# Kernel optimization log

Measured on AMD Instinct MI355X. Metric: run time of the kernel, lower is better.

## Reference

```python
import jax, jax.numpy as jnp
import numpy as np

V, D, H, L, T_CTX = 50257, 768, 12, 12, 1024
HD = D // H
GELU_C = float(np.sqrt(2.0 / np.pi))


def new_gelu(x):
    return 0.5 * x * (1.0 + jnp.tanh(GELU_C * (x + 0.044715 * x ** 3)))


def layernorm(x, w, b, eps=1e-5):
    mu = jnp.mean(x, axis=-1, keepdims=True)
    var = jnp.var(x, axis=-1, keepdims=True)
    return (x - mu) * jax.lax.rsqrt(var + eps) * w + b


def setup_inputs() -> dict:
    key = jax.random.key(0)
    ks = jax.random.split(key, 20)
    B, T = 2, 1024
    s = 0.02
    inp = {
        "idx": jax.random.randint(ks[0], (B, T), 0, V),
        "targets": jax.random.randint(ks[1], (B, T), 0, V),
        "wte": jax.random.normal(ks[2], (V, D), jnp.float32) * s,
        "wpe": jax.random.normal(ks[3], (T_CTX, D), jnp.float32) * s,
        "ln1_w": jnp.ones((L, D)), "ln1_b": jnp.zeros((L, D)),
        "qkv_w": jax.random.normal(ks[4], (L, D, 3 * D), jnp.float32) * s,
        "qkv_b": jnp.zeros((L, 3 * D)),
        "proj_w": jax.random.normal(ks[5], (L, D, D), jnp.float32) * s,
        "proj_b": jnp.zeros((L, D)),
        "ln2_w": jnp.ones((L, D)), "ln2_b": jnp.zeros((L, D)),
        "fc_w": jax.random.normal(ks[6], (L, D, 4 * D), jnp.float32) * s,
        "fc_b": jnp.zeros((L, 4 * D)),
        "fc2_w": jax.random.normal(ks[7], (L, 4 * D, D), jnp.float32) * s,
        "fc2_b": jnp.zeros((L, D)),
        "lnf_w": jnp.ones((D,)), "lnf_b": jnp.zeros((D,)),
    }
    return inp


def _gpt_forward(idx, targets, wte, wpe, ln1_w, ln1_b, qkv_w, qkv_b, proj_w,
                 proj_b, ln2_w, ln2_b, fc_w, fc_b, fc2_w, fc2_b, lnf_w, lnf_b):
    B, T = idx.shape
    x = wte[idx] + wpe[:T]  # [B,T,D]
    scale = 1.0 / np.sqrt(HD)
    causal = jnp.tril(jnp.ones((T, T), dtype=bool))

    def block(x, p):
        l1w, l1b, qw, qb, pw, pb, l2w, l2b, fw, fb, f2w, f2b = p
        h = layernorm(x, l1w, l1b)
        qkv = h @ qw + qb  # [B,T,3D]
        q, k, v = jnp.split(qkv, 3, axis=-1)
        q = q.reshape(B, T, H, HD).transpose(0, 2, 1, 3)
        k = k.reshape(B, T, H, HD).transpose(0, 2, 1, 3)
        v = v.reshape(B, T, H, HD).transpose(0, 2, 1, 3)
        attn = jnp.einsum('bhqd,bhkd->bhqk', q, k) * scale
        attn = jnp.where(causal, attn, -jnp.inf)
        attn = jax.nn.softmax(attn, axis=-1)
        o = jnp.einsum('bhqk,bhkd->bhqd', attn, v)
        o = o.transpose(0, 2, 1, 3).reshape(B, T, D)
        x = x + (o @ pw + pb)
        h = layernorm(x, l2w, l2b)
        h = new_gelu(h @ fw + fb) @ f2w + f2b
        return x + h, None

    params = (ln1_w, ln1_b, qkv_w, qkv_b, proj_w, proj_b,
              ln2_w, ln2_b, fc_w, fc_b, fc2_w, fc2_b)
    x, _ = jax.lax.scan(block, x, params)
    x = layernorm(x, lnf_w, lnf_b)
    logits = x @ wte.T  # tied lm_head, [B,T,V]

    logp = jax.nn.log_softmax(logits, axis=-1)
    tflat = targets.reshape(-1)
    valid = tflat != -1
    tsafe = jnp.where(valid, tflat, 0)
    nll = -jnp.take_along_axis(logp.reshape(-1, V), tsafe[:, None], axis=-1)[:, 0]
    loss = jnp.sum(jnp.where(valid, nll, 0.0)) / jnp.maximum(jnp.sum(valid), 1)
    return logits, loss


def reference(idx, targets, wte, wpe, ln1_w, ln1_b, qkv_w, qkv_b, proj_w,
              proj_b, ln2_w, ln2_b, fc_w, fc_b, fc2_w, fc2_b, lnf_w, lnf_b):
    return _gpt_forward(idx, targets, wte, wpe, ln1_w, ln1_b, qkv_w, qkv_b,
                        proj_w, proj_b, ln2_w, ln2_b, fc_w, fc_b, fc2_w, fc2_b,
                        lnf_w, lnf_b)
```

## Files before the change

### kernel.cpp

```cpp
#include <hip/hip_runtime.h>
#include <hip/hip_bf16.h>
#include <math.h>

#define TT 1024
#define BB 2
#define DD 768
#define HH 12
#define NHD 64
#define LL 12
#define VV 50257
#define MROWS (BB*TT)
#define VPAD 50304
#define NT 393
#define NROWS (MROWS*HH)

typedef __attribute__((ext_vector_type(4))) float f32x4;
typedef __attribute__((ext_vector_type(8))) __bf16 bf16x8;
typedef __attribute__((ext_vector_type(8))) unsigned short u16x8;
typedef __hip_bfloat16 bf16;

__device__ __forceinline__ void gload_lds16(const bf16* g, bf16* l) {
    __builtin_amdgcn_global_load_lds((const __attribute__((address_space(1))) void*)g,
                                     (__attribute__((address_space(3))) void*)l, 16, 0, 0);
}

__global__ void embed_kernel(const int* __restrict__ idx, const float* __restrict__ wte,
                             const float* __restrict__ wpe, float* __restrict__ x) {
    int m = blockIdx.x;
    int t = m % TT;
    int tok = idx[m];
    const float* wrow = wte + (size_t)tok * DD;
    const float* prow = wpe + (size_t)t * DD;
    float* xrow = x + (size_t)m * DD;
    for (int c = threadIdx.x; c < DD; c += blockDim.x)
        xrow[c] = wrow[c] + prow[c];
}

__global__ void ln_kernel(const float* __restrict__ x, const float* __restrict__ w,
                          const float* __restrict__ b, bf16* __restrict__ out) {
    __shared__ float red[256];
    int m = blockIdx.x;
    int tid = threadIdx.x;
    const float* xr = x + (size_t)m * DD;
    float v0 = xr[tid], v1 = xr[tid + 256], v2 = xr[tid + 512];
    red[tid] = v0 + v1 + v2;
    __syncthreads();
    for (int s = 128; s > 0; s >>= 1) { if (tid < s) red[tid] += red[tid + s]; __syncthreads(); }
    float mu = red[0] * (1.0f / DD);
    __syncthreads();
    float d0 = v0 - mu, d1 = v1 - mu, d2 = v2 - mu;
    red[tid] = d0 * d0 + d1 * d1 + d2 * d2;
    __syncthreads();
    for (int s = 128; s > 0; s >>= 1) { if (tid < s) red[tid] += red[tid + s]; __syncthreads(); }
    float rstd = rsqrtf(red[0] * (1.0f / DD) + 1e-5f);
    bf16* orow = out + (size_t)m * DD;
    orow[tid]       = __float2bfloat16(d0 * rstd * w[tid]       + b[tid]);
    orow[tid + 256] = __float2bfloat16(d1 * rstd * w[tid + 256] + b[tid + 256]);
    orow[tid + 512] = __float2bfloat16(d2 * rstd * w[tid + 512] + b[tid + 512]);
}

__global__ void redln_kernel(const float* __restrict__ part, const float* __restrict__ bias,
                             const float* __restrict__ w, const float* __restrict__ b,
                             float* __restrict__ x, bf16* __restrict__ hb) {
    __shared__ float red[256];
    const size_t MN = (size_t)MROWS * DD;
    int m = blockIdx.x;
    int tid = threadIdx.x;
    float v[3];
    #pragma unroll
    for (int j = 0; j < 3; ++j) {
        int c = tid + j * 256;
        size_t i = (size_t)m * DD + c;
        v[j] = x[i] + part[i] + part[MN + i] + bias[c];
        x[i] = v[j];
    }
    red[tid] = v[0] + v[1] + v[2];
    __syncthreads();
    for (int s = 128; s > 0; s >>= 1) { if (tid < s) red[tid] += red[tid + s]; __syncthreads(); }
    float mu = red[0] * (1.0f / DD);
    __syncthreads();
    float d0 = v[0] - mu, d1 = v[1] - mu, d2 = v[2] - mu;
    red[tid] = d0 * d0 + d1 * d1 + d2 * d2;
    __syncthreads();
    for (int s = 128; s > 0; s >>= 1) { if (tid < s) red[tid] += red[tid + s]; __syncthreads(); }
    float rstd = rsqrtf(red[0] * (1.0f / DD) + 1e-5f);
    bf16* orow = hb + (size_t)m * DD;
    orow[tid]       = __float2bfloat16(d0 * rstd * w[tid]       + b[tid]);
    orow[tid + 256] = __float2bfloat16(d1 * rstd * w[tid + 256] + b[tid + 256]);
    orow[tid + 512] = __float2bfloat16(d2 * rstd * w[tid + 512] + b[tid + 512]);
}

__global__ void cast_kernel(const float* __restrict__ src, bf16* __restrict__ dst, int n4) {
    int stride = gridDim.x * blockDim.x;
    for (int i = blockIdx.x * blockDim.x + threadIdx.x; i < n4; i += stride) {
        float4 v = *(const float4*)(src + (size_t)i * 4);
        bf16* d = dst + (size_t)i * 4;
        d[0] = __float2bfloat16(v.x); d[1] = __float2bfloat16(v.y);
        d[2] = __float2bfloat16(v.z); d[3] = __float2bfloat16(v.w);
    }
}

__global__ void padzero_kernel(bf16* __restrict__ p, int n) {
    int i = blockIdx.x * 256 + threadIdx.x;
    if (i < n) p[i] = __float2bfloat16(0.f);
}

__global__ void tcast_kernel(const float* __restrict__ W, bf16* __restrict__ Wt,
                             int K, int N, size_t wstride, size_t tstride) {
    W  += (size_t)blockIdx.z * wstride;
    Wt += (size_t)blockIdx.z * tstride;
    __shared__ float t[32][33];
    int n0 = blockIdx.x * 32, k0 = blockIdx.y * 32;
    int c = threadIdx.x & 31, g = threadIdx.x >> 5;
    #pragma unroll
    for (int i = 0; i < 4; ++i) {
        int k = g * 4 + i;
        t[k][c] = W[(size_t)(k0 + k) * N + n0 + c];
    }
    __syncthreads();
    #pragma unroll
    for (int i = 0; i < 4; ++i) {
        int n = g * 4 + i;
        Wt[(size_t)(n0 + n) * K + k0 + c] = __float2bfloat16(t[c][n]);
    }
}

template<int BM, int BN, bool BIAS, bool GELU_, bool RES, bool OUTBF16, bool SPLITK>
__global__ __launch_bounds__(256, 3) void mgemm(
        const bf16* __restrict__ A, const bf16* __restrict__ Bm,
        const float* __restrict__ bias, const float* __restrict__ res,
        float* __restrict__ Cf, bf16* __restrict__ Cb, int M, int N, int K) {
    constexpr int WM = BM / 32, WN = BN / 32;
    constexpr int RA = BM / 32, RB = BN / 32;
    constexpr int NL = RA + RB;
    __shared__ __align__(16) bf16 As[2][BM * 64];
    __shared__ __align__(16) bf16 Bs[2][BN * 64];
    const int tid = threadIdx.x, lane = tid & 63, wid = tid >> 6;
    const int nbx = gridDim.x;
    const int nwg = nbx * gridDim.y;
    const int bidl = blockIdx.x + nbx * blockIdx.y;
    const int cpx = nwg >> 3;
    const int sw = (bidl & 7) * cpx + (bidl >> 3);
    const int m0 = (sw % nbx) * BM, n0 = (sw / nbx) * BN;
    const int wr = (wid >> 1) * (BM / 2), wc = (wid & 1) * (BN / 2);
    const int fr = lane & 15, fq = lane >> 4;

    const int Keff  = SPLITK ? (K >> 1) : K;
    const int kbase = SPLITK ? blockIdx.z * Keff : 0;
    if (SPLITK) Cf += (size_t)blockIdx.z * M * N;

    const int srow = tid >> 3;
    const int sk   = ((tid & 7) ^ (srow & 7)) * 8;
    const bf16* gA = A  + (size_t)(m0 + srow) * K + kbase + sk;
    const bf16* gB = Bm + (size_t)(n0 + srow) * K + kbase + sk;

    const int nt = Keff / 64;
    f32x4 acc[WM][WN] = {};

    auto stage = [&](int t) {
        bf16* dA = &As[t & 1][0] + tid * 8;
        bf16* dB = &Bs[t & 1][0] + tid * 8;
        const bf16* pA = gA + t * 64;
        const bf16* pB = gB + t * 64;
        #pragma unroll
        for (int u = 0; u < RA; ++u) gload_lds16(pA + (size_t)(u * 32) * K, dA + u * 2048);
        #pragma unroll
        for (int u = 0; u < RB; ++u) gload_lds16(pB + (size_t)(u * 32) * K, dB + u * 2048);
    };

    stage(0);

    for (int t = 0; t < nt; ++t) {
        if (t + 1 < nt) {
            stage(t + 1);
            asm volatile("s_waitcnt vmcnt(%0)" :: "i"(NL) : "memory");
        } else {
            asm volatile("s_waitcnt vmcnt(0)" ::: "memory");
        }
        __builtin_amdgcn_s_barrier();
        __builtin_amdgcn_sched_barrier(0);
        const bf16* abase = &As[t & 1][0];
        const bf16* bbase = &Bs[t & 1][0];
        #pragma unroll
        for (int ks = 0; ks < 2; ++ks) {
            const int kp = ((ks * 4 + fq) ^ (fr & 7)) * 8;
            bf16x8 af[WM], bq[WN];
            #pragma unroll
            for (int m = 0; m < WM; ++m)
                af[m] = *(const bf16x8*)(abase + (wr + m * 16 + fr) * 64 + kp);
            #pragma unroll
            for (int n = 0; n < WN; ++n)
                bq[n] = *(const bf16x8*)(bbase + (wc + n * 16 + fr) * 64 + kp);
            #pragma unroll
            for (int m = 0; m < WM; ++m)
                #pragma unroll
                for (int n = 0; n < WN; ++n)
                    acc[m][n] = __builtin_amdgcn_mfma_f32_16x16x32_bf16(af[m], bq[n], acc[m][n], 0, 0, 0);
        }
        __builtin_amdgcn_sched_barrier(0);
        __builtin_amdgcn_s_barrier();
    }

    #pragma unroll
    for (int m = 0; m < WM; ++m) {
        const int row = m0 + wr + m * 16 + fq * 4;
        #pragma unroll
        for (int n = 0; n < WN; ++n) {
            const int col = n0 + wc + n * 16 + fr;
            float bv = BIAS ? bias[col] : 0.f;
            #pragma unroll
            for (int r = 0; r < 4; ++r) {
                float v = acc[m][n][r] + bv;
                if (GELU_) {
                    float u = v;
                    float z = 1.5957691216057308f * (u + 0.044715f * u * u * u);
                    v = u / (1.0f + __expf(-z));
                }
                if (RES) v += res[(size_t)(row + r) * N + col];
                if (OUTBF16) Cb[(size_t)(row + r) * N + col] = __float2bfloat16(v);
                else         Cf[(size_t)(row + r) * N + col] = v;
            }
        }
    }
}

__global__ __launch_bounds__(512, 4) void mgemmL(
        const bf16* __restrict__ A, const bf16* __restrict__ Bm,
        float* __restrict__ Cf, float2* __restrict__ P, int N, int K) {
    constexpr int NL = 3;
    __shared__ __align__(16) bf16 As[2][256 * 32];
    __shared__ __align__(16) bf16 Bs[2][128 * 32];
    __shared__ float2 lbuf[8][64];
    const int tid = threadIdx.x, lane = tid & 63, wid = tid >> 6;
    const int nbx = gridDim.x;
    const int nwg = nbx * gridDim.y;
    const int bidl = blockIdx.x + nbx * blockIdx.y;
    const int cpx = nwg >> 3;
    const int sw = (bidl & 7) * cpx + (bidl >> 3);
    const int m0 = (sw % nbx) * 256, n0 = (sw / nbx) * 128;
    const int wm = wid >> 1, wn = wid & 1;
    const int wr = wm * 64, wc = wn * 64;
    const int fr = lane & 15, fq = lane >> 4;

    const int srow = tid >> 2;
    const int ksrc = ((tid & 3) ^ ((tid >> 3) & 3)) * 8;
    const bf16* gA = A  + (size_t)(m0 + srow) * K + ksrc;
    const bf16* gB = Bm + (size_t)(n0 + srow) * K + ksrc;
    const int kph = (fq ^ ((fr >> 1) & 3)) * 8;

    f32x4 acc[4][4] = {};
    const int nt = K / 32;

    auto stage = [&](int t) {
        bf16* dA = &As[t & 1][0] + tid * 8;
        bf16* dB = &Bs[t & 1][0] + tid * 8;
        const bf16* pA = gA + t * 32;
        #pragma unroll
        for (int u = 0; u < 2; ++u) gload_lds16(pA + (size_t)(u * 128) * K, dA + u * 4096);
        gload_lds16(gB + t * 32, dB);
    };

    stage(0);

    for (int t = 0; t < nt; ++t) {
        if (t + 1 < nt) {
            stage(t + 1);
            asm volatile("s_waitcnt vmcnt(%0)" :: "i"(NL) : "memory");
        } else {
            asm volatile("s_waitcnt vmcnt(0)" ::: "memory");
        }
        __builtin_amdgcn_s_barrier();
        __builtin_amdgcn_sched_barrier(0);
        const bf16* abase = &As[t & 1][0];
        const bf16* bbase = &Bs[t & 1][0];
        bf16x8 af[4], bq[4];
        #pragma unroll
        for (int m = 0; m < 4; ++m)
            af[m] = *(const bf16x8*)(abase + (wr + m * 16 + fr) * 32 + kph);
        #pragma unroll
        for (int n = 0; n < 4; ++n)
            bq[n] = *(const bf16x8*)(bbase + (wc + n * 16 + fr) * 32 + kph);
        #pragma unroll
        for (int m = 0; m < 4; ++m)
            #pragma unroll
            for (int n = 0; n < 4; ++n)
                acc[m][n] = __builtin_amdgcn_mfma_f32_16x16x32_bf16(af[m], bq[n], acc[m][n], 0, 0, 0);
        __builtin_amdgcn_sched_barrier(0);
        __builtin_amdgcn_s_barrier();
    }

    #pragma unroll
    for (int m = 0; m < 4; ++m) {
        const int row = m0 + wr + m * 16 + fq * 4;
        #pragma unroll
        for (int n = 0; n < 4; ++n) {
            const int col = n0 + wc + n * 16 + fr;
            if (col < N) {
                #pragma unroll
                for (int r = 0; r < 4; ++r)
                    Cf[(size_t)(row + r) * N + col] = acc[m][n][r];
            }
        }
    }
    #pragma unroll
    for (int m = 0; m < 4; ++m) {
        #pragma unroll
        for (int r = 0; r < 4; ++r) {
            float mx = -1e30f;
            #pragma unroll
            for (int n = 0; n < 4; ++n) {
                int col = n0 + wc + n * 16 + fr;
                mx = fmaxf(mx, (col < N) ? acc[m][n][r] : -1e30f);
            }
            #pragma unroll
            for (int msk = 1; msk <= 8; msk <<= 1) mx = fmaxf(mx, __shfl_xor(mx, msk));
            float sm = 0.f;
            #pragma unroll
            for (int n = 0; n < 4; ++n) {
                int col = n0 + wc + n * 16 + fr;
                if (col < N) sm += __expf(acc[m][n][r] - mx);
            }
            #pragma unroll
            for (int msk = 1; msk <= 8; msk <<= 1) sm += __shfl_xor(sm, msk);
            if (fr == 0) lbuf[wid][m * 16 + fq * 4 + r] = make_float2(mx, sm);
        }
    }
    __syncthreads();
    if (tid < 256) {
        int band = tid >> 6, rl = tid & 63;
        float2 a = lbuf[band * 2][rl];
        float2 b = lbuf[band * 2 + 1][rl];
        float mc = fmaxf(a.x, b.x);
        float sc = a.y * __expf(a.x - mc) + b.y * __expf(b.x - mc);
        P[(size_t)(m0 + band * 64 + rl) * NT + (n0 >> 7)] = make_float2(mc, sc);
    }
}

__global__ __launch_bounds__(256) void attn3_kernel(const bf16* __restrict__ qkv,
                                                    float* __restrict__ po,
                                                    float2* __restrict__ pml) {
    __shared__ bf16 Vt[64 * 64];
    __shared__ bf16 Ps[4][16 * 64];
    const int bid = blockIdx.x;
    const int z = blockIdx.y;
    const int q0 = (15 - (bid & 15)) * 64;
    const int h  = (bid / (TT / 64)) % HH;
    const int b  = bid / ((TT / 64) * HH);
    const int tid = threadIdx.x, lane = tid & 63, wid = tid >> 6;
    const int fr = lane & 15, fq = lane >> 4;
    const size_t rs = 3 * DD;

    const int nt_all = q0 / 64 + 1;
    const int lo = z ? (nt_all + 1) / 2 : 0;
    const int hi = z ? nt_all : (nt_all + 1) / 2;

    po  += (size_t)z * MROWS * DD;
    pml += (size_t)z * NROWS;

    if (lo >= hi) {
        #pragma unroll
        for (int r = 0; r < 4; ++r) {
            int q = q0 + wid * 16 + fq * 4 + r;
            size_t pidx = ((size_t)(b * TT + q) * HH + h);
            #pragma unroll
            for (int n2 = 0; n2 < 4; ++n2)
                po[pidx * NHD + n2 * 16 + fr] = 0.f;
            if (fr == 0) pml[pidx] = make_float2(-1e30f, 0.f);
        }
        return;
    }

    bf16x8 qf[2];
    {
        const bf16* qb = qkv + (size_t)(b * TT + q0 + wid * 16 + fr) * rs + h * NHD;
        qf[0] = *(const bf16x8*)(qb + fq * 8);
        qf[1] = *(const bf16x8*)(qb + 32 + fq * 8);
    }
    float mrun[4] = {-1e30f, -1e30f, -1e30f, -1e30f};
    float lrun[4] = {0.f, 0.f, 0.f, 0.f};
    f32x4 o[4] = {};
    const int vrow = (tid & 31) * 2, kq = tid >> 5;

    for (int jt = lo; jt < hi; ++jt) {
        __syncthreads();
        {
            const u16x8* vb = (const u16x8*)(qkv + (size_t)(b * TT + jt * 64 + vrow) * rs + 2 * DD + h * NHD + kq * 8);
            u16x8 v0 = vb[0];
            u16x8 v1 = *(const u16x8*)((const bf16*)vb + rs);
            #pragma unroll
            for (int j = 0; j < 8; ++j) {
                int d = kq * 8 + j;
                int e = (d * 64 + vrow) ^ ((d & 7) << 3);
                *(unsigned int*)&Vt[e] = (unsigned int)v0[j] | ((unsigned int)v1[j] << 16);
            }
        }
        f32x4 s[4] = {};
        const bf16* kb = qkv + (size_t)(b * TT + jt * 64 + fr) * rs + DD + h * NHD;
        __builtin_amdgcn_s_setprio(1);
        #pragma unroll
        for (int n = 0; n < 4; ++n) {
            bf16x8 k0 = *(const bf16x8*)(kb + (size_t)(n * 16) * rs + fq * 8);
            bf16x8 k1 = *(const bf16x8*)(kb + (size_t)(n * 16) * rs + 32 + fq * 8);
            s[n] = __builtin_amdgcn_mfma_f32_16x16x32_bf16(qf[0], k0, s[n], 0, 0, 0);
            s[n] = __builtin_amdgcn_mfma_f32_16x16x32_bf16(qf[1], k1, s[n], 0, 0, 0);
        }
        __builtin_amdgcn_s_setprio(0);
        float mt[4] = {-1e30f, -1e30f, -1e30f, -1e30f};
        #pragma unroll
        for (int n = 0; n < 4; ++n) {
            int colg = jt * 64 + n * 16 + fr;
            #pragma unroll
            for (int r = 0; r < 4; ++r) {
                int rowg = q0 + wid * 16 + fq * 4 + r;
                float v = s[n][r] * 0.125f;
                if (colg > rowg) v = -1e30f;
                s[n][r] = v;
                mt[r] = fmaxf(mt[r], v);
            }
        }
        #pragma unroll
        for (int msk = 1; msk <= 8; msk <<= 1)
            #pragma unroll
            for (int r = 0; r < 4; ++r) mt[r] = fmaxf(mt[r], __shfl_xor(mt[r], msk));
        float sc[4], pt[4] = {0.f, 0.f, 0.f, 0.f};
        #pragma unroll
        for (int r = 0; r < 4; ++r) {
            float mn = fmaxf(mrun[r], mt[r]);
            sc[r] = __expf(mrun[r] - mn);
            mrun[r] = mn;
        }
        #pragma unroll
        for (int n = 0; n < 4; ++n)
            #pragma unroll
            for (int r = 0; r < 4; ++r) {
                float p = __expf(s[n][r] - mrun[r]);
                s[n][r] = p;
                pt[r] += p;
            }
        #pragma unroll
        for (int msk = 1; msk <= 8; msk <<= 1)
            #pragma unroll
            for (int r = 0; r < 4; ++r) pt[r] += __shfl_xor(pt[r], msk);
        #pragma unroll
        for (int r = 0; r < 4; ++r) lrun[r] = lrun[r] * sc[r] + pt[r];
        #pragma unroll
        for (int n2 = 0; n2 < 4; ++n2)
            #pragma unroll
            for (int r = 0; r < 4; ++r) o[n2][r] *= sc[r];
        #pragma unroll
        for (int n = 0; n < 4; ++n)
            #pragma unroll
            for (int r = 0; r < 4; ++r) {
                int row = fq * 4 + r;
                int e = (row * 64 + n * 16 + fr) ^ ((row & 7) << 3);
                Ps[wid][e] = __float2bfloat16(s[n][r]);
            }
        __syncthreads();
        __builtin_amdgcn_s_setprio(1);
        #pragma unroll
        for (int ks = 0; ks < 2; ++ks) {
            int pe = (fr * 64 + ks * 32 + fq * 8) ^ ((fr & 7) << 3);
            bf16x8 pa = *(const bf16x8*)&Ps[wid][pe];
            #pragma unroll
            for (int n2 = 0; n2 < 4; ++n2) {
                int d = n2 * 16 + fr;
                int ve = (d * 64 + ks * 32 + fq * 8) ^ ((d & 7) << 3);
                bf16x8 vv = *(const bf16x8*)&Vt[ve];
                o[n2] = __builtin_amdgcn_mfma_f32_16x16x32_bf16(pa, vv, o[n2], 0, 0, 0);
            }
        }
        __builtin_amdgcn_s_setprio(0);
    }
    #pragma unroll
    for (int r = 0; r < 4; ++r) {
        int q = q0 + wid * 16 + fq * 4 + r;
        size_t pidx = ((size_t)(b * TT + q) * HH + h);
        #pragma unroll
        for (int n2 = 0; n2 < 4; ++n2)
            po[pidx * NHD + n2 * 16 + fr] = o[n2][r];
        if (fr == 0) pml[pidx] = make_float2(mrun[r], lrun[r]);
    }
}

__global__ void attn_combine(const float* __restrict__ po, const float2* __restrict__ pml,
                             bf16* __restrict__ out) {
    const size_t ZO = (size_t)MROWS * DD;
    int tid = threadIdx.x;
    size_t pidx = (size_t)blockIdx.x * 4 + (tid >> 6);
    int d = tid & 63;
    float2 a = pml[pidx];
    float2 b = pml[NROWS + pidx];
    float mt = fmaxf(a.x, b.x);
    float e0 = __expf(a.x - mt), e1 = __expf(b.x - mt);
    float l = a.y * e0 + b.y * e1;
    float ov = po[pidx * NHD + d] * e0 + po[ZO + pidx * NHD + d] * e1;
    int h = (int)(pidx % HH);
    size_t bt = pidx / HH;
    out[bt * DD + h * NHD + d] = __float2bfloat16(ov / l);
}

__global__ void zero_kernel(float* p) { if (threadIdx.x == 0) p[0] = 0.f; }

__global__ void loss_finish(const float2* __restrict__ P, const float* __restrict__ logits,
                            const int* __restrict__ targets, float* __restrict__ acc) {
    __shared__ float rm[256], rs[256];
    int m = blockIdx.x;
    int tid = threadIdx.x;
    float mx = -1e30f, sm = 0.f;
    for (int i = tid; i < NT; i += 256) {
        float2 p = P[(size_t)m * NT + i];
        float nm = fmaxf(mx, p.x);
        sm = sm * __expf(mx - nm) + p.y * __expf(p.x - nm);
        mx = nm;
    }
    rm[tid] = mx; rs[tid] = sm;
    __syncthreads();
    for (int s = 128; s > 0; s >>= 1) {
        if (tid < s) {
            float m2 = rm[tid + s], s2 = rs[tid + s];
            float nm = fmaxf(rm[tid], m2);
            rs[tid] = rs[tid] * __expf(rm[tid] - nm) + s2 * __expf(m2 - nm);
            rm[tid] = nm;
        }
        __syncthreads();
    }
    if (tid == 0) {
        float lse = logf(rs[0]) + rm[0];
        atomicAdd(acc, lse - logits[(size_t)m * VV + targets[m]]);
    }
}

__global__ void loss_final(const float* __restrict__ acc, float* __restrict__ out) {
    if (threadIdx.x == 0) out[0] = acc[0] * (1.0f / (float)MROWS);
}

extern "C" void kernel_launch(void* const* d_in, const int* in_sizes, int n_in,
                              void* d_out, int out_size, void* d_ws, size_t ws_size,
                              hipStream_t stream) {
    const int*   idx     = (const int*)d_in[0];
    const int*   targets = (const int*)d_in[1];
    const float* wte     = (const float*)d_in[2];
    const float* wpe     = (const float*)d_in[3];
    const float* ln1_w   = (const float*)d_in[4];
    const float* ln1_b   = (const float*)d_in[5];
    const float* qkv_w   = (const float*)d_in[6];
    const float* qkv_b   = (const float*)d_in[7];
    const float* proj_w  = (const float*)d_in[8];
    const float* proj_b  = (const float*)d_in[9];
    const float* ln2_w   = (const float*)d_in[10];
    const float* ln2_b   = (const float*)d_in[11];
    const float* fc_w    = (const float*)d_in[12];
    const float* fc_b    = (const float*)d_in[13];
    const float* fc2_w   = (const float*)d_in[14];
    const float* fc2_b   = (const float*)d_in[15];
    const float* lnf_w   = (const float*)d_in[16];
    const float* lnf_b   = (const float*)d_in[17];

    float* logits = (float*)d_out;
    float* loss_out = logits + (size_t)MROWS * VV;

    const size_t LQ = (size_t)3 * DD * DD, LP = (size_t)DD * DD;
    const size_t LF = (size_t)4 * DD * DD, LF2 = (size_t)4 * DD * DD;
    const size_t LSTRIDE = LQ + LP + LF + LF2;

    float* x    = (float*)d_ws;
    float* lacc = x + (size_t)MROWS * DD;
    float* part = lacc + 16;
    float2* pml = (float2*)(part + (size_t)2 * MROWS * DD);
    bf16* qkvbuf = (bf16*)(pml + (size_t)2 * NROWS);
    bf16* hb   = qkvbuf + (size_t)MROWS * 3 * DD;
    bf16* ab   = hb + (size_t)MROWS * DD;
    bf16* gb   = ab + (size_t)MROWS * DD;
    bf16* wteb = gb + (size_t)MROWS * 4 * DD;
    bf16* wbase = wteb + (size_t)VPAD * DD;

    const size_t fixed_bytes = (size_t)((char*)wbase - (char*)d_ws);
    const bool hoist = ws_size >= fixed_bytes + sizeof(bf16) * LSTRIDE * LL;

    dim3 blk(256);
    cast_kernel<<<2048, blk, 0, stream>>>(wte, wteb, VV * DD / 4);
    padzero_kernel<<<((VPAD - VV) * DD + 255) / 256, blk, 0, stream>>>(
        wteb + (size_t)VV * DD, (VPAD - VV) * DD);
    embed_kernel<<<MROWS, blk, 0, stream>>>(idx, wte, wpe, x);

    if (hoist) {
        tcast_kernel<<<dim3(3 * DD / 32, DD / 32, LL), blk, 0, stream>>>(
            qkv_w, wbase, DD, 3 * DD, LQ, LSTRIDE);
        tcast_kernel<<<dim3(DD / 32, DD / 32, LL), blk, 0, stream>>>(
            proj_w, wbase + LQ, DD, DD, LP, LSTRIDE);
        tcast_kernel<<<dim3(4 * DD / 32, DD / 32, LL), blk, 0, stream>>>(
            fc_w, wbase + LQ + LP, DD, 4 * DD, LF, LSTRIDE);
        tcast_kernel<<<dim3(DD / 32, 4 * DD / 32, LL), blk, 0, stream>>>(
            fc2_w, wbase + LQ + LP + LF, 4 * DD, DD, LF2, LSTRIDE);
    }

    ln_kernel<<<MROWS, blk, 0, stream>>>(x, ln1_w, ln1_b, hb);

    for (int l = 0; l < LL; ++l) {
        bf16* wl = hoist ? wbase + (size_t)l * LSTRIDE : wbase;
        bf16* wQT = wl, *wPT = wl + LQ, *wFT = wl + LQ + LP, *wF2T = wl + LQ + LP + LF;
        if (!hoist) {
            tcast_kernel<<<dim3(3 * DD / 32, DD / 32, 1), blk, 0, stream>>>(qkv_w + (size_t)l * LQ, wQT, DD, 3 * DD, 0, 0);
            tcast_kernel<<<dim3(DD / 32, DD / 32, 1), blk, 0, stream>>>(proj_w + (size_t)l * LP, wPT, DD, DD, 0, 0);
            tcast_kernel<<<dim3(4 * DD / 32, DD / 32, 1), blk, 0, stream>>>(fc_w + (size_t)l * LF, wFT, DD, 4 * DD, 0, 0);
            tcast_kernel<<<dim3(DD / 32, 4 * DD / 32, 1), blk, 0, stream>>>(fc2_w + (size_t)l * LF2, wF2T, 4 * DD, DD, 0, 0);
        }

        mgemm<128, 64, true, false, false, true, false><<<dim3(MROWS / 128, 3 * DD / 64), blk, 0, stream>>>(
            hb, wQT, qkv_b + (size_t)l * 3 * DD, nullptr, nullptr, qkvbuf, MROWS, 3 * DD, DD);

        attn3_kernel<<<dim3(BB * HH * (TT / 64), 2), blk, 0, stream>>>(qkvbuf, part, pml);
        attn_combine<<<NROWS / 4, blk, 0, stream>>>(part, pml, ab);

        mgemm<64, 64, false, false, false, false, true><<<dim3(MROWS / 64, DD / 64, 2), blk, 0, stream>>>(
            ab, wPT, nullptr, nullptr, part, nullptr, MROWS, DD, DD);
        redln_kernel<<<MROWS, blk, 0, stream>>>(part, proj_b + (size_t)l * DD,
            ln2_w + (size_t)l * DD, ln2_b + (size_t)l * DD, x, hb);

        mgemm<128, 64, true, true, false, true, false><<<dim3(MROWS / 128, 4 * DD / 64), blk, 0, stream>>>(
            hb, wFT, fc_b + (size_t)l * 4 * DD, nullptr, nullptr, gb, MROWS, 4 * DD, DD);

        mgemm<64, 64, false, false, false, false, true><<<dim3(MROWS / 64, DD / 64, 2), blk, 0, stream>>>(
            gb, wF2T, nullptr, nullptr, part, nullptr, MROWS, DD, 4 * DD);
        const float* nw = (l + 1 < LL) ? ln1_w + (size_t)(l + 1) * DD : lnf_w;
        const float* nb = (l + 1 < LL) ? ln1_b + (size_t)(l + 1) * DD : lnf_b;
        redln_kernel<<<MROWS, blk, 0, stream>>>(part, fc2_b + (size_t)l * DD, nw, nb, x, hb);
    }

    mgemmL<<<dim3(MROWS / 256, VPAD / 128), dim3(512), 0, stream>>>(
        hb, wteb, logits, (float2*)part, VV, DD);

    zero_kernel<<<1, 64, 0, stream>>>(lacc);
    loss_finish<<<MROWS, blk, 0, stream>>>((const float2*)part, logits, targets, lacc);
    loss_final<<<1, 64, 0, stream>>>(lacc, loss_out);
}
```

Measured before the change: 2.185 ms.

## Fuse attention split-KV combine into projection GEMM A-operand staging

Removes the separate attn_combine kernel and instead merges the two partial attention outputs (with their max/sum rescaling) while loading the A tile of a new projection GEMM kernel, writing bf16 directly into LDS. This skips a kernel launch and the round trip through the bf16 attention buffer. In exchange, each GEMM block re-reads fp32 partials from both splits and recomputes the softmax rescale factors, and the A tile is now staged with register loads instead of direct-to-LDS loads. A separate po buffer is added so the attention partials no longer alias the projection output partials.

New measurement: 2.289 ms. +4.7%, slower.

```diff
diff --git a/kernel.cpp b/kernel.cpp
--- a/kernel.cpp
+++ b/kernel.cpp
@@ -224,6 +224,117 @@
     }
 }
 
+__global__ __launch_bounds__(256, 3) void mgemmP(
+        const float* __restrict__ po, const float2* __restrict__ pml,
+        const bf16* __restrict__ Bm, float* __restrict__ Cf) {
+    constexpr int BM = 64, BN = 64;
+    constexpr int M = MROWS, N = DD, K = DD;
+    __shared__ __align__(16) bf16 As[2][BM * 64];
+    __shared__ __align__(16) bf16 Bs[2][BN * 64];
+    const int tid = threadIdx.x, lane = tid & 63, wid = tid >> 6;
+    const int nbx = gridDim.x;
+    const int nwg = nbx * gridDim.y;
+    const int bidl = blockIdx.x + nbx * blockIdx.y;
+    const int cpx = nwg >> 3;
+    const int sw = (bidl & 7) * cpx + (bidl >> 3);
+    const int m0 = (sw % nbx) * BM, n0 = (sw / nbx) * BN;
+    const int wr = (wid >> 1) * 32, wc = (wid & 1) * 32;
+    const int fr = lane & 15, fq = lane >> 4;
+
+    const int Keff = K >> 1;
+    const int kbase = blockIdx.z * Keff;
+    Cf += (size_t)blockIdx.z * (size_t)M * N;
+
+    const int srow = tid >> 3;
+    const int sk   = ((tid & 7) ^ (srow & 7)) * 8;
+    const bf16* gB = Bm + (size_t)(n0 + srow) * K + kbase + sk;
+    const size_t ZO = (size_t)MROWS * DD;
+    const int h0 = kbase >> 6;
+
+    const int nt = Keff / 64;
+    f32x4 acc[2][2] = {};
+
+    auto stageB = [&](int t) {
+        bf16* dB = &Bs[t & 1][0] + tid * 8;
+        const bf16* pB = gB + t * 64;
+        #pragma unroll
+        for (int u = 0; u < 2; ++u) gload_lds16(pB + (size_t)(u * 32) * K, dB + u * 2048);
+    };
+    auto stageA = [&](int t) {
+        bf16* dA = &As[t & 1][0] + tid * 8;
+        const int h = h0 + t;
+        #pragma unroll
+        for (int u = 0; u < 2; ++u) {
+            const int row = m0 + srow + u * 32;
+            const size_t pidx = (size_t)row * HH + h;
+            f32x4 a0 = *(const f32x4*)(po + pidx * NHD + sk);
+            f32x4 a1 = *(const f32x4*)(po + pidx * NHD + sk + 4);
+            f32x4 b0 = *(const f32x4*)(po + ZO + pidx * NHD + sk);
+            f32x4 b1 = *(const f32x4*)(po + ZO + pidx * NHD + sk + 4);
+            float2 ml0 = pml[pidx];
+            float2 ml1 = pml[NROWS + pidx];
+            float mt = fmaxf(ml0.x, ml1.x);
+            float e0 = __expf(ml0.x - mt), e1 = __expf(ml1.x - mt);
+            float inv = 1.f / (ml0.y * e0 + ml1.y * e1);
+            e0 *= inv; e1 *= inv;
+            union { bf16x8 v; bf16 h8[8]; } o;
+            #pragma unroll
+            for (int j = 0; j < 4; ++j) {
+                o.h8[j]     = __float2bfloat16(a0[j] * e0 + b0[j] * e1);
+                o.h8[j + 4] = __float2bfloat16(a1[j] * e0 + b1[j] * e1);
+            }
+            *(bf16x8*)(dA + u * 2048) = o.v;
+        }
+    };
+
+    stageB(0); stageA(0);
+
+    for (int t = 0; t < nt; ++t) {
+        if (t + 1 < nt) {
+            stageB(t + 1);
+            stageA(t + 1);
+            asm volatile("s_waitcnt vmcnt(2)" ::: "memory");
+        } else {
+            asm volatile("s_waitcnt vmcnt(0)" ::: "memory");
+        }
+        asm volatile("s_waitcnt lgkmcnt(0)" ::: "memory");
+        __builtin_amdgcn_s_barrier();
+        __builtin_amdgcn_sched_barrier(0);
+        const bf16* abase = &As[t & 1][0];
+        const bf16* bbase = &Bs[t & 1][0];
+        #pragma unroll
+        for (int ks = 0; ks < 2; ++ks) {
+            const int kp = ((ks * 4 + fq) ^ (fr & 7)) * 8;
+            bf16x8 af[2], bq[2];
+            #pragma unroll
+            for (int m = 0; m < 2; ++m)
+                af[m] = *(const bf16x8*)(abase + (wr + m * 16 + fr) * 64 + kp);
+            #pragma unroll
+            for (int n = 0; n < 2; ++n)
+                bq[n] = *(const bf16x8*)(bbase + (wc + n * 16 + fr) * 64 + kp);
+            #pragma unroll
+            for (int m = 0; m < 2; ++m)
+                #pragma unroll
+                for (int n = 0; n < 2; ++n)
+                    acc[m][n] = __builtin_amdgcn_mfma_f32_16x16x32_bf16(af[m], bq[n], acc[m][n], 0, 0, 0);
+        }
+        __builtin_amdgcn_sched_barrier(0);
+        __builtin_amdgcn_s_barrier();
+    }
+
+    #pragma unroll
+    for (int m = 0; m < 2; ++m) {
+        const int row = m0 + wr + m * 16 + fq * 4;
+        #pragma unroll
+        for (int n = 0; n < 2; ++n) {
+            const int col = n0 + wc + n * 16 + fr;
+            #pragma unroll
+            for (int r = 0; r < 4; ++r)
+                Cf[(size_t)(row + r) * N + col] = acc[m][n][r];
+        }
+    }
+}
+
 __global__ __launch_bounds__(512, 4) void mgemmL(
         const bf16* __restrict__ A, const bf16* __restrict__ Bm,
         float* __restrict__ Cf, float2* __restrict__ P, int N, int K) {
@@ -480,23 +591,6 @@
             po[pidx * NHD + n2 * 16 + fr] = o[n2][r];
         if (fr == 0) pml[pidx] = make_float2(mrun[r], lrun[r]);
     }
-}
-
-__global__ void attn_combine(const float* __restrict__ po, const float2* __restrict__ pml,
-                             bf16* __restrict__ out) {
-    const size_t ZO = (size_t)MROWS * DD;
-    int tid = threadIdx.x;
-    size_t pidx = (size_t)blockIdx.x * 4 + (tid >> 6);
-    int d = tid & 63;
-    float2 a = pml[pidx];
-    float2 b = pml[NROWS + pidx];
-    float mt = fmaxf(a.x, b.x);
-    float e0 = __expf(a.x - mt), e1 = __expf(b.x - mt);
-    float l = a.y * e0 + b.y * e1;
-    float ov = po[pidx * NHD + d] * e0 + po[ZO + pidx * NHD + d] * e1;
-    int h = (int)(pidx % HH);
-    size_t bt = pidx / HH;
-    out[bt * DD + h * NHD + d] = __float2bfloat16(ov / l);
 }
 
 __global__ void zero_kernel(float* p) { if (threadIdx.x == 0) p[0] = 0.f; }
@@ -566,11 +660,11 @@
     float* x    = (float*)d_ws;
     float* lacc = x + (size_t)MROWS * DD;
     float* part = lacc + 16;
-    float2* pml = (float2*)(part + (size_t)2 * MROWS * DD);
+    float* po   = part + (size_t)2 * MROWS * DD;
+    float2* pml = (float2*)(po + (size_t)2 * MROWS * DD);
     bf16* qkvbuf = (bf16*)(pml + (size_t)2 * NROWS);
     bf16* hb   = qkvbuf + (size_t)MROWS * 3 * DD;
-    bf16* ab   = hb + (size_t)MROWS * DD;
-    bf16* gb   = ab + (size_t)MROWS * DD;
+    bf16* gb   = hb + (size_t)MROWS * DD;
     bf16* wteb = gb + (size_t)MROWS * 4 * DD;
     bf16* wbase = wteb + (size_t)VPAD * DD;
 
@@ -609,11 +703,9 @@
         mgemm<128, 64, true, false, false, true, false><<<dim3(MROWS / 128, 3 * DD / 64), blk, 0, stream>>>(
             hb, wQT, qkv_b + (size_t)l * 3 * DD, nullptr, nullptr, qkvbuf, MROWS, 3 * DD, DD);
 
-        attn3_kernel<<<dim3(BB * HH * (TT / 64), 2), blk, 0, stream>>>(qkvbuf, part, pml);
-        attn_combine<<<NROWS / 4, blk, 0, stream>>>(part, pml, ab);
-
-        mgemm<64, 64, false, false, false, false, true><<<dim3(MROWS / 64, DD / 64, 2), blk, 0, stream>>>(
-            ab, wPT, nullptr, nullptr, part, nullptr, MROWS, DD, DD);
+        attn3_kernel<<<dim3(BB * HH * (TT / 64), 2), blk, 0, stream>>>(qkvbuf, po, pml);
+
+        mgemmP<<<dim3(MROWS / 64, DD / 64, 2), blk, 0, stream>>>(po, pml, wPT, part);
         redln_kernel<<<MROWS, blk, 0, stream>>>(part, proj_b + (size_t)l * DD,
             ln2_w + (size_t)l * DD, ln2_b + (size_t)l * DD, x, hb);
 
```
